# Kernel optimization log

Measured on AMD Instinct MI355X. Metric: run time of the kernel, lower is better.

Reference implementation:

```python
import jax, jax.numpy as jnp
from jax import lax
import numpy as np

B, N, H, K = 64, 256, 1024, 3  # batch, num_proposals, hidden_dim, conv kernel size
LN_EPS = 1e-5


def setup_inputs() -> dict:
    key = jax.random.key(0)
    k1, k2, k3 = jax.random.split(key, 3)
    scale = 1.0 / np.sqrt(H)
    return {
        "f": jax.random.normal(k1, (B, N, H), dtype=jnp.float32),
        "k": jax.random.normal(k2, (B, N, H), dtype=jnp.float32),
        "W_lin": jax.random.normal(k3, (N * K, H), dtype=jnp.float32) * scale,
        "b_lin": jnp.zeros((N * K,), dtype=jnp.float32),
        "ln_gamma": jnp.ones((H,), dtype=jnp.float32),
        "ln_beta": jnp.zeros((H,), dtype=jnp.float32),
    }


def _conv_one(x, w):
    # x: [N, H] (channels, length); w: [N_out, N_in, K]
    # PyTorch F.conv1d is cross-correlation, same as lax conv with no flip.
    y = lax.conv_general_dilated(
        x[None], w, window_strides=(1,), padding="SAME",
        dimension_numbers=("NCH", "OIH", "NCH"))
    return y[0]  # [N, H]


def reference(f, k, W_lin, b_lin, ln_gamma, ln_beta):
    # Dynamic weight generation: [B, N, H] -> [B, N, N*K] -> [B, N, N, K]
    weight = jnp.einsum("bnh,oh->bno", f, W_lin) + b_lin
    weight = weight.reshape(B, N, N, K)
    # Per-sample dynamic conv1d over the hidden dim (batched via vmap)
    out = jax.vmap(_conv_one)(k, weight)  # [B, N, H]
    # LayerNorm over hidden dim
    mu = jnp.mean(out, axis=-1, keepdims=True)
    var = jnp.var(out, axis=-1, keepdims=True)
    out = (out - mu) * lax.rsqrt(var + LN_EPS) * ln_gamma + ln_beta
    return out
```

## Files before the change

### kernel.cpp

```cpp
#include <hip/hip_runtime.h>
#include <math.h>

#define Bsz 64
#define Nn  256
#define Hh  1024
#define NK  768

typedef __bf16 bf16;
typedef bf16 bf16x4 __attribute__((ext_vector_type(4)));
typedef bf16 bf16x8 __attribute__((ext_vector_type(8)));
typedef float floatx4 __attribute__((ext_vector_type(4)));

#define KT_ROWS   1026
#define KT_BSTRIDE (KT_ROWS * 256)

__device__ __forceinline__ void gl_lds16(const bf16* g, bf16* l) {
    __builtin_amdgcn_global_load_lds(
        (__attribute__((address_space(1))) void*)(g),
        (__attribute__((address_space(3))) void*)(l), 16, 0, 0);
}
__device__ __forceinline__ void gl_lds16f(const float* g, float* l) {
    __builtin_amdgcn_global_load_lds(
        (__attribute__((address_space(1))) void*)(g),
        (__attribute__((address_space(3))) void*)(l), 16, 0, 0);
}

__global__ __launch_bounds__(256) void transpose_kernel(
    const float* __restrict__ kin, bf16* __restrict__ kTp)
{
    __shared__ float Tf[64 * 128];
    const int tid = threadIdx.x;
    const int bid = blockIdx.x;
    const int hb = bid & 7, ib = (bid >> 3) & 3, b = bid >> 5;
    const int i0 = ib * 64, h0 = hb * 128;
    const float* src = kin + ((size_t)b << 18);
    bf16* dstb = kTp + (size_t)b * KT_BSTRIDE;

    if (hb == 0 && ib == 0) {
        dstb[tid] = (bf16)0.f;
        dstb[(size_t)1025 * 256 + tid] = (bf16)0.f;
    }
    #pragma unroll
    for (int j = 0; j < 8; ++j) {
        int c  = tid + j * 256;
        int il = c >> 5;
        int hq = (c & 31) ^ j;
        gl_lds16f(src + (size_t)(i0 + il) * Hh + h0 + hq * 4, Tf + c * 4);
    }
    __syncthreads();
    const int q = tid & 7;
    #pragma unroll
    for (int p = 0; p < 4; ++p) {
        int hl = (tid >> 3) + p * 32;
        bf16x8 o;
        #pragma unroll
        for (int j = 0; j < 8; ++j) {
            int i = q * 8 + j;
            float v = Tf[i * 128 + (((hl >> 2) ^ q) << 2) + (hl & 3)];
            o[j] = (bf16)v;
        }
        *(bf16x8*)&dstb[(size_t)(h0 + hl + 1) * 256 + i0 + q * 8] = o;
    }
}

__global__ __launch_bounds__(256) void gemm1_mfma(
    const float* __restrict__ A,
    const float* __restrict__ Bw,
    const float* __restrict__ bias,
    bf16* __restrict__ wgt3)
{
    __shared__ bf16 smem[25600];
    const int tid  = threadIdx.x;
    const int wave = tid >> 6, lane = tid & 63;
    const int bid = blockIdx.x;
    const int xcd = bid & 7, loc = bid >> 3;
    const int ry  = (xcd << 4) | (loc >> 2);
    const int cx  = loc & 3;
    const int row0 = ry * 128;
    const int col0 = cx * 192;

    size_t offA[8];
    #pragma unroll
    for (int j = 0; j < 8; ++j) {
        int c = tid + j * 256, row = c >> 4, kq = c & 15;
        offA[j] = (size_t)(row0 + row) * Hh + kq * 4;
    }
    size_t offB[12];
    #pragma unroll
    for (int j = 0; j < 12; ++j) {
        int c = tid + j * 256, row = c >> 4, kq = c & 15;
        offB[j] = (size_t)(col0 + row) * Hh + kq * 4;
    }

    const int wm = wave & 1, wn = wave >> 1;
    const int fm = lane & 15, koct = (lane >> 4) * 8;

    floatx4 zero = {0.f, 0.f, 0.f, 0.f};
    floatx4 acc[4][6];
    #pragma unroll
    for (int i = 0; i < 4; ++i)
        #pragma unroll
        for (int j = 0; j < 6; ++j) acc[i][j] = zero;

    for (int k0 = 0; k0 < Hh; k0 += 64) {
        float4 av[8];
        #pragma unroll
        for (int j = 0; j < 8; ++j) av[j] = *(const float4*)&A[offA[j] + k0];
        float4 bv[12];
        #pragma unroll
        for (int j = 0; j < 12; ++j) bv[j] = *(const float4*)&Bw[offB[j] + k0];
        __syncthreads();
        #pragma unroll
        for (int j = 0; j < 8; ++j) {
            int c = tid + j * 256;
            bf16x4 o = {(bf16)av[j].x, (bf16)av[j].y, (bf16)av[j].z, (bf16)av[j].w};
            *(bf16x4*)&smem[c * 4] = o;
        }
        #pragma unroll
        for (int j = 0; j < 12; ++j) {
            int c = tid + j * 256;
            bf16x4 o = {(bf16)bv[j].x, (bf16)bv[j].y, (bf16)bv[j].z, (bf16)bv[j].w};
            *(bf16x4*)&smem[8192 + c * 4] = o;
        }
        __syncthreads();
        #pragma unroll
        for (int q = 0; q < 2; ++q) {
            bf16x8 af[4], bfr[6];
            #pragma unroll
            for (int mt = 0; mt < 4; ++mt)
                af[mt] = *(const bf16x8*)&smem[(wm * 64 + mt * 16 + fm) * 64 + q * 32 + koct];
            #pragma unroll
            for (int nt = 0; nt < 6; ++nt)
                bfr[nt] = *(const bf16x8*)&smem[8192 + (wn * 96 + nt * 16 + fm) * 64 + q * 32 + koct];
            #pragma unroll
            for (int mt = 0; mt < 4; ++mt)
                #pragma unroll
                for (int nt = 0; nt < 6; ++nt)
                    acc[mt][nt] = __builtin_amdgcn_mfma_f32_16x16x32_bf16(
                        af[mt], bfr[nt], acc[mt][nt], 0, 0, 0);
        }
    }
    __syncthreads();

    const int b  = row0 >> 8;
    const int nb = row0 & 255;
    bf16* Cs = smem;
    #pragma unroll
    for (int nt = 0; nt < 6; ++nt) {
        int c = wn * 96 + nt * 16 + fm;
        float bl = bias[col0 + c];
        #pragma unroll
        for (int mt = 0; mt < 4; ++mt) {
            int rb = wm * 64 + mt * 16 + (lane >> 4) * 4;
            #pragma unroll
            for (int r = 0; r < 4; ++r)
                Cs[(rb + r) * 200 + c] = (bf16)(acc[mt][nt][r] + bl);
        }
    }
    __syncthreads();
    const int i0 = cx * 64;
    #pragma unroll
    for (int j = 0; j < 12; ++j) {
        int s = tid + j * 256;
        int t = s >> 10, rem = s & 1023, n = rem >> 3, q8 = rem & 7;
        bf16x8 v;
        #pragma unroll
        for (int u = 0; u < 8; ++u)
            v[u] = Cs[n * 200 + (q8 * 8 + u) * 3 + t];
        *(bf16x8*)&wgt3[((size_t)(b * 3 + t) << 16) + ((size_t)(nb + n) << 8) + i0 + q8 * 8] = v;
    }
}

__global__ __launch_bounds__(256) void conv_mfma(
    const bf16* __restrict__ kTp,
    const bf16* __restrict__ wgt3,
    bf16* __restrict__ cbuf)
{
    __shared__ bf16 As[6144];
    __shared__ bf16 Ks[4160];
    const int tid  = threadIdx.x;
    const int wave = tid >> 6, lane = tid & 63;
    const int bid = blockIdx.x;
    const int xcd = bid & 7, loc = bid >> 3;
    const int b   = (xcd << 3) | (loc >> 5);
    const int rem = loc & 31;
    const int o0  = (rem >> 3) * 64;
    const int h0  = (rem & 7) * 128;
    const int wm = wave & 1, wn = wave >> 1;
    const int fm = lane & 15, koct = (lane >> 4) * 8;

    const bf16* gA[3]; bf16* lA[3];
    #pragma unroll
    for (int j = 0; j < 3; ++j) {
        int s = tid + j * 256;
        int t = s >> 8, r2 = s & 255, o = r2 >> 2, iq = r2 & 3;
        gA[j] = wgt3 + ((size_t)(b * 3 + t) << 16) + ((size_t)(o0 + o) << 8) + iq * 8;
        lA[j] = As + s * 8;
    }
    const bf16* kb = kTp + (size_t)b * KT_BSTRIDE;
    const bf16* gK[2]; bf16* lK[2];
    #pragma unroll
    for (int j = 0; j < 2; ++j) {
        int s = tid + j * 256;
        int r = s >> 2, quad = s & 3;
        gK[j] = kb + (size_t)(h0 + r) * 256 + quad * 8;
        lK[j] = Ks + s * 8;
    }
    const bf16* gH = kb + (size_t)(h0 + 128 + (tid >> 2)) * 256 + (tid & 3) * 8;
    const int lH = (128 + (tid >> 2)) * 32 + (tid & 3) * 8;

    floatx4 zero = {0.f, 0.f, 0.f, 0.f};
    floatx4 acc[2][4];
    #pragma unroll
    for (int i = 0; i < 2; ++i)
        #pragma unroll
        for (int j = 0; j < 4; ++j) acc[i][j] = zero;

    for (int ic = 0; ic < 8; ++ic) {
        const int i0 = ic * 32;
        __syncthreads();
        #pragma unroll
        for (int j = 0; j < 3; ++j) gl_lds16(gA[j] + i0, lA[j]);
        #pragma unroll
        for (int j = 0; j < 2; ++j) gl_lds16(gK[j] + i0, lK[j]);
        if (tid < 8) {
            bf16x8 v = *(const bf16x8*)(gH + i0);
            *(bf16x8*)&Ks[lH] = v;
        }
        __syncthreads();
        #pragma unroll
        for (int t = 0; t < 3; ++t) {
            bf16x8 af[2], bfr[4];
            #pragma unroll
            for (int mt = 0; mt < 2; ++mt)
                af[mt] = *(const bf16x8*)&As[t * 2048 + (wm * 32 + mt * 16 + fm) * 32 + koct];
            #pragma unroll
            for (int nt = 0; nt < 4; ++nt)
                bfr[nt] = *(const bf16x8*)&Ks[(wn * 64 + nt * 16 + fm + t) * 32 + koct];
            #pragma unroll
            for (int mt = 0; mt < 2; ++mt)
                #pragma unroll
                for (int nt = 0; nt < 4; ++nt)
                    acc[mt][nt] = __builtin_amdgcn_mfma_f32_16x16x32_bf16(
                        af[mt], bfr[nt], acc[mt][nt], 0, 0, 0);
        }
    }

    #pragma unroll
    for (int mt = 0; mt < 2; ++mt) {
        int o = o0 + wm * 32 + mt * 16 + (lane >> 4) * 4;
        #pragma unroll
        for (int nt = 0; nt < 4; ++nt) {
            int h = h0 + wn * 64 + nt * 16 + fm;
            #pragma unroll
            for (int r = 0; r < 4; ++r)
                cbuf[((size_t)(b * 256 + o + r) << 10) + h] = (bf16)acc[mt][nt][r];
        }
    }
}

__global__ __launch_bounds__(256) void ln_kernel(
    const bf16* __restrict__ cbuf, const float* __restrict__ gamma,
    const float* __restrict__ beta, float* __restrict__ out)
{
    const int tid  = threadIdx.x;
    const int t    = tid & 127;
    const int half = tid >> 7;
    bf16x8 v[4];
    #pragma unroll
    for (int it = 0; it < 4; ++it) {
        const int row = (blockIdx.x << 3) + it * 2 + half;
        v[it] = *(const bf16x8*)(cbuf + ((size_t)row << 10) + t * 8);
    }
    float4 g0  = ((const float4*)gamma)[t * 2];
    float4 g1  = ((const float4*)gamma)[t * 2 + 1];
    float4 be0 = ((const float4*)beta)[t * 2];
    float4 be1 = ((const float4*)beta)[t * 2 + 1];
    __shared__ float r1[2][4], r2[2][4];
    #pragma unroll
    for (int it = 0; it < 4; ++it) {
        const int row = (blockIdx.x << 3) + it * 2 + half;
        float x[8];
        float s1 = 0.f, s2 = 0.f;
        #pragma unroll
        for (int u = 0; u < 8; ++u) {
            x[u] = (float)v[it][u];
            s1 += x[u];
            s2 += x[u] * x[u];
        }
        #pragma unroll
        for (int m = 1; m < 64; m <<= 1) {
            s1 += __shfl_xor(s1, m, 64);
            s2 += __shfl_xor(s2, m, 64);
        }
        const int p = it & 1;
        if ((tid & 63) == 0) { r1[p][tid >> 6] = s1; r2[p][tid >> 6] = s2; }
        __syncthreads();
        float S1 = r1[p][2 * half] + r1[p][2 * half + 1];
        float S2 = r2[p][2 * half] + r2[p][2 * half + 1];
        float mu   = S1 * (1.0f / 1024.0f);
        float var  = S2 * (1.0f / 1024.0f) - mu * mu;
        float rstd = rsqrtf(var + 1e-5f);
        float4 o0, o1;
        o0.x = (x[0] - mu) * rstd * g0.x + be0.x;
        o0.y = (x[1] - mu) * rstd * g0.y + be0.y;
        o0.z = (x[2] - mu) * rstd * g0.z + be0.z;
        o0.w = (x[3] - mu) * rstd * g0.w + be0.w;
        o1.x = (x[4] - mu) * rstd * g1.x + be1.x;
        o1.y = (x[5] - mu) * rstd * g1.y + be1.y;
        o1.z = (x[6] - mu) * rstd * g1.z + be1.z;
        o1.w = (x[7] - mu) * rstd * g1.w + be1.w;
        float* orow = out + ((size_t)row << 10) + t * 8;
        ((float4*)orow)[0] = o0;
        ((float4*)orow)[1] = o1;
    }
}

extern "C" void kernel_launch(void* const* d_in, const int* in_sizes, int n_in,
                              void* d_out, int out_size, void* d_ws, size_t ws_size,
                              hipStream_t stream) {
    const float* f     = (const float*)d_in[0];
    const float* kin   = (const float*)d_in[1];
    const float* W_lin = (const float*)d_in[2];
    const float* b_lin = (const float*)d_in[3];
    const float* gamma = (const float*)d_in[4];
    const float* beta  = (const float*)d_in[5];
    float* out = (float*)d_out;

    char* ws = (char*)d_ws;
    bf16* cbuf = (bf16*)(ws);
    bf16* kTp  = (bf16*)(ws + 35127296);
    bf16* wgt3 = (bf16*)(ws + 68747264);

    transpose_kernel<<<2048, 256, 0, stream>>>(kin, kTp);
    gemm1_mfma<<<512, 256, 0, stream>>>(f, W_lin, b_lin, wgt3);
    conv_mfma<<<2048, 256, 0, stream>>>(kTp, wgt3, cbuf);
    ln_kernel<<<2048, 256, 0, stream>>>(cbuf, gamma, beta, out);
}
```

Measured before the change: 259.8 us.

## Double-buffer gemm1 LDS with register prefetch and halve the output tile

The weight-generation GEMM now uses a 128x96 output tile instead of 128x192, doubling the grid to 1024 blocks. The K loop steps by 32 instead of 64 and uses two LDS buffers: the next slice is prefetched into registers while MFMAs run on the current buffer, then stored to the other buffer, so each step needs one barrier instead of two. LDS rows are padded to a stride of 40 to reduce bank conflicts. Smaller tiles mean more global reloads of the A operand across column blocks, traded for better occupancy and latency hiding.

```diff
diff --git a/kernel.cpp b/kernel.cpp
--- a/kernel.cpp
+++ b/kernel.cpp
@@ -69,104 +69,123 @@
     const float* __restrict__ bias,
     bf16* __restrict__ wgt3)
 {
-    __shared__ bf16 smem[25600];
+    __shared__ bf16 smem[17920];
     const int tid  = threadIdx.x;
     const int wave = tid >> 6, lane = tid & 63;
     const int bid = blockIdx.x;
     const int xcd = bid & 7, loc = bid >> 3;
-    const int ry  = (xcd << 4) | (loc >> 2);
-    const int cx  = loc & 3;
+    const int ry  = (xcd << 4) | (loc >> 3);
+    const int cx  = loc & 7;
     const int row0 = ry * 128;
-    const int col0 = cx * 192;
-
-    size_t offA[8];
-    #pragma unroll
-    for (int j = 0; j < 8; ++j) {
-        int c = tid + j * 256, row = c >> 4, kq = c & 15;
-        offA[j] = (size_t)(row0 + row) * Hh + kq * 4;
-    }
-    size_t offB[12];
-    #pragma unroll
-    for (int j = 0; j < 12; ++j) {
-        int c = tid + j * 256, row = c >> 4, kq = c & 15;
-        offB[j] = (size_t)(col0 + row) * Hh + kq * 4;
+    const int col0 = cx * 96;
+
+    const float* gA[4]; int lA[4];
+    #pragma unroll
+    for (int j = 0; j < 4; ++j) {
+        int c = tid + j * 256, row = c >> 3, kq = c & 7;
+        gA[j] = A + (size_t)(row0 + row) * Hh + kq * 4;
+        lA[j] = row * 40 + kq * 4;
+    }
+    const float* gB[3]; int lB[3];
+    #pragma unroll
+    for (int j = 0; j < 3; ++j) {
+        int c = tid + j * 256, row = c >> 3, kq = c & 7;
+        gB[j] = Bw + (size_t)(col0 + row) * Hh + kq * 4;
+        lB[j] = 5120 + row * 40 + kq * 4;
     }
 
     const int wm = wave & 1, wn = wave >> 1;
     const int fm = lane & 15, koct = (lane >> 4) * 8;
 
     floatx4 zero = {0.f, 0.f, 0.f, 0.f};
-    floatx4 acc[4][6];
+    floatx4 acc[4][3];
     #pragma unroll
     for (int i = 0; i < 4; ++i)
         #pragma unroll
-        for (int j = 0; j < 6; ++j) acc[i][j] = zero;
-
-    for (int k0 = 0; k0 < Hh; k0 += 64) {
-        float4 av[8];
-        #pragma unroll
-        for (int j = 0; j < 8; ++j) av[j] = *(const float4*)&A[offA[j] + k0];
-        float4 bv[12];
-        #pragma unroll
-        for (int j = 0; j < 12; ++j) bv[j] = *(const float4*)&Bw[offB[j] + k0];
+        for (int j = 0; j < 3; ++j) acc[i][j] = zero;
+
+    float4 av[4]; float4 bv[3];
+    #pragma unroll
+    for (int j = 0; j < 4; ++j) av[j] = *(const float4*)(gA[j]);
+    #pragma unroll
+    for (int j = 0; j < 3; ++j) bv[j] = *(const float4*)(gB[j]);
+    #pragma unroll
+    for (int j = 0; j < 4; ++j) {
+        bf16x4 o = {(bf16)av[j].x, (bf16)av[j].y, (bf16)av[j].z, (bf16)av[j].w};
+        *(bf16x4*)&smem[lA[j]] = o;
+    }
+    #pragma unroll
+    for (int j = 0; j < 3; ++j) {
+        bf16x4 o = {(bf16)bv[j].x, (bf16)bv[j].y, (bf16)bv[j].z, (bf16)bv[j].w};
+        *(bf16x4*)&smem[lB[j]] = o;
+    }
+    __syncthreads();
+
+    int cur = 0;
+    for (int ks = 0; ks < 32; ++ks) {
+        if (ks < 31) {
+            const int ko = (ks + 1) * 32;
+            #pragma unroll
+            for (int j = 0; j < 4; ++j) av[j] = *(const float4*)(gA[j] + ko);
+            #pragma unroll
+            for (int j = 0; j < 3; ++j) bv[j] = *(const float4*)(gB[j] + ko);
+        }
+        const int cb = cur * 8960;
+        bf16x8 af[4], bfr[3];
+        #pragma unroll
+        for (int mt = 0; mt < 4; ++mt)
+            af[mt] = *(const bf16x8*)&smem[cb + (wm * 64 + mt * 16 + fm) * 40 + koct];
+        #pragma unroll
+        for (int nt = 0; nt < 3; ++nt)
+            bfr[nt] = *(const bf16x8*)&smem[cb + 5120 + (wn * 48 + nt * 16 + fm) * 40 + koct];
+        #pragma unroll
+        for (int mt = 0; mt < 4; ++mt)
+            #pragma unroll
+            for (int nt = 0; nt < 3; ++nt)
+                acc[mt][nt] = __builtin_amdgcn_mfma_f32_16x16x32_bf16(
+                    af[mt], bfr[nt], acc[mt][nt], 0, 0, 0);
+        if (ks < 31) {
+            const int ob = (cur ^ 1) * 8960;
+            #pragma unroll
+            for (int j = 0; j < 4; ++j) {
+                bf16x4 o = {(bf16)av[j].x, (bf16)av[j].y, (bf16)av[j].z, (bf16)av[j].w};
+                *(bf16x4*)&smem[ob + lA[j]] = o;
+            }
+            #pragma unroll
+            for (int j = 0; j < 3; ++j) {
+                bf16x4 o = {(bf16)bv[j].x, (bf16)bv[j].y, (bf16)bv[j].z, (bf16)bv[j].w};
+                *(bf16x4*)&smem[ob + lB[j]] = o;
+            }
+        }
         __syncthreads();
-        #pragma unroll
-        for (int j = 0; j < 8; ++j) {
-            int c = tid + j * 256;
-            bf16x4 o = {(bf16)av[j].x, (bf16)av[j].y, (bf16)av[j].z, (bf16)av[j].w};
-            *(bf16x4*)&smem[c * 4] = o;
-        }
-        #pragma unroll
-        for (int j = 0; j < 12; ++j) {
-            int c = tid + j * 256;
-            bf16x4 o = {(bf16)bv[j].x, (bf16)bv[j].y, (bf16)bv[j].z, (bf16)bv[j].w};
-            *(bf16x4*)&smem[8192 + c * 4] = o;
-        }
-        __syncthreads();
-        #pragma unroll
-        for (int q = 0; q < 2; ++q) {
-            bf16x8 af[4], bfr[6];
-            #pragma unroll
-            for (int mt = 0; mt < 4; ++mt)
-                af[mt] = *(const bf16x8*)&smem[(wm * 64 + mt * 16 + fm) * 64 + q * 32 + koct];
-            #pragma unroll
-            for (int nt = 0; nt < 6; ++nt)
-                bfr[nt] = *(const bf16x8*)&smem[8192 + (wn * 96 + nt * 16 + fm) * 64 + q * 32 + koct];
-            #pragma unroll
-            for (int mt = 0; mt < 4; ++mt)
-                #pragma unroll
-                for (int nt = 0; nt < 6; ++nt)
-                    acc[mt][nt] = __builtin_amdgcn_mfma_f32_16x16x32_bf16(
-                        af[mt], bfr[nt], acc[mt][nt], 0, 0, 0);
-        }
-    }
-    __syncthreads();
+        cur ^= 1;
+    }
 
     const int b  = row0 >> 8;
     const int nb = row0 & 255;
     bf16* Cs = smem;
     #pragma unroll
-    for (int nt = 0; nt < 6; ++nt) {
-        int c = wn * 96 + nt * 16 + fm;
+    for (int nt = 0; nt < 3; ++nt) {
+        int c = wn * 48 + nt * 16 + fm;
         float bl = bias[col0 + c];
         #pragma unroll
         for (int mt = 0; mt < 4; ++mt) {
             int rb = wm * 64 + mt * 16 + (lane >> 4) * 4;
             #pragma unroll
             for (int r = 0; r < 4; ++r)
-                Cs[(rb + r) * 200 + c] = (bf16)(acc[mt][nt][r] + bl);
+                Cs[(rb + r) * 104 + c] = (bf16)(acc[mt][nt][r] + bl);
         }
     }
     __syncthreads();
-    const int i0 = cx * 64;
-    #pragma unroll
-    for (int j = 0; j < 12; ++j) {
+    const int i0 = cx * 32;
+    #pragma unroll
+    for (int j = 0; j < 6; ++j) {
         int s = tid + j * 256;
-        int t = s >> 10, rem = s & 1023, n = rem >> 3, q8 = rem & 7;
+        int t = s >> 9, rem = s & 511, n = rem >> 2, q8 = rem & 3;
         bf16x8 v;
         #pragma unroll
         for (int u = 0; u < 8; ++u)
-            v[u] = Cs[n * 200 + (q8 * 8 + u) * 3 + t];
+            v[u] = Cs[n * 104 + (q8 * 8 + u) * 3 + t];
         *(bf16x8*)&wgt3[((size_t)(b * 3 + t) << 16) + ((size_t)(nb + n) << 8) + i0 + q8 * 8] = v;
     }
 }
@@ -333,7 +352,7 @@
     bf16* wgt3 = (bf16*)(ws + 68747264);
 
     transpose_kernel<<<2048, 256, 0, stream>>>(kin, kTp);
-    gemm1_mfma<<<512, 256, 0, stream>>>(f, W_lin, b_lin, wgt3);
+    gemm1_mfma<<<1024, 256, 0, stream>>>(f, W_lin, b_lin, wgt3);
     conv_mfma<<<2048, 256, 0, stream>>>(kTp, wgt3, cbuf);
     ln_kernel<<<2048, 256, 0, stream>>>(cbuf, gamma, beta, out);
 }
```

Measured after the change: 284.7 us. 9.6% more time.

## Prefetch next K-tile into registers and pad LDS rows in gemm1

Applied to the files above, without the earlier changes.

Restructures the gemm1 main loop so the global loads for the next 64-wide K slice are issued before the MFMA work on the current slice. This hides global memory latency behind compute at the cost of holding more live registers. It also pads the LDS row stride from 64 to 72 bf16 and changes the epilogue stride from 200 to 194, both meant to cut LDS bank conflicts. The LDS footprint grows, and the added registers could reduce occupancy.

```diff
diff --git a/kernel.cpp b/kernel.cpp
--- a/kernel.cpp
+++ b/kernel.cpp
@@ -79,17 +79,19 @@
     const int row0 = ry * 128;
     const int col0 = cx * 192;
 
-    size_t offA[8];
+    const float* gA[8]; int lA[8];
     #pragma unroll
     for (int j = 0; j < 8; ++j) {
         int c = tid + j * 256, row = c >> 4, kq = c & 15;
-        offA[j] = (size_t)(row0 + row) * Hh + kq * 4;
-    }
-    size_t offB[12];
+        gA[j] = A + (size_t)(row0 + row) * Hh + kq * 4;
+        lA[j] = row * 72 + kq * 4;
+    }
+    const float* gB[12]; int lB[12];
     #pragma unroll
     for (int j = 0; j < 12; ++j) {
         int c = tid + j * 256, row = c >> 4, kq = c & 15;
-        offB[j] = (size_t)(col0 + row) * Hh + kq * 4;
+        gB[j] = Bw + (size_t)(col0 + row) * Hh + kq * 4;
+        lB[j] = 9216 + row * 72 + kq * 4;
     }
 
     const int wm = wave & 1, wn = wave >> 1;
@@ -102,36 +104,41 @@
         #pragma unroll
         for (int j = 0; j < 6; ++j) acc[i][j] = zero;
 
-    for (int k0 = 0; k0 < Hh; k0 += 64) {
-        float4 av[8];
-        #pragma unroll
-        for (int j = 0; j < 8; ++j) av[j] = *(const float4*)&A[offA[j] + k0];
-        float4 bv[12];
-        #pragma unroll
-        for (int j = 0; j < 12; ++j) bv[j] = *(const float4*)&Bw[offB[j] + k0];
-        __syncthreads();
-        #pragma unroll
-        for (int j = 0; j < 8; ++j) {
-            int c = tid + j * 256;
-            bf16x4 o = {(bf16)av[j].x, (bf16)av[j].y, (bf16)av[j].z, (bf16)av[j].w};
-            *(bf16x4*)&smem[c * 4] = o;
-        }
-        #pragma unroll
-        for (int j = 0; j < 12; ++j) {
-            int c = tid + j * 256;
-            bf16x4 o = {(bf16)bv[j].x, (bf16)bv[j].y, (bf16)bv[j].z, (bf16)bv[j].w};
-            *(bf16x4*)&smem[8192 + c * 4] = o;
-        }
-        __syncthreads();
+    float4 av[8]; float4 bv[12];
+    #pragma unroll
+    for (int j = 0; j < 8; ++j) av[j] = *(const float4*)(gA[j]);
+    #pragma unroll
+    for (int j = 0; j < 12; ++j) bv[j] = *(const float4*)(gB[j]);
+    #pragma unroll
+    for (int j = 0; j < 8; ++j) {
+        bf16x4 o = {(bf16)av[j].x, (bf16)av[j].y, (bf16)av[j].z, (bf16)av[j].w};
+        *(bf16x4*)&smem[lA[j]] = o;
+    }
+    #pragma unroll
+    for (int j = 0; j < 12; ++j) {
+        bf16x4 o = {(bf16)bv[j].x, (bf16)bv[j].y, (bf16)bv[j].z, (bf16)bv[j].w};
+        *(bf16x4*)&smem[lB[j]] = o;
+    }
+    __syncthreads();
+
+    for (int ks = 0; ks < 16; ++ks) {
+        if (ks < 15) {
+            const int ko = (ks + 1) * 64;
+            #pragma unroll
+            for (int j = 0; j < 8; ++j) av[j] = *(const float4*)(gA[j] + ko);
+            #pragma unroll
+            for (int j = 0; j < 12; ++j) bv[j] = *(const float4*)(gB[j] + ko);
+            __builtin_amdgcn_sched_barrier(0);
+        }
         #pragma unroll
         for (int q = 0; q < 2; ++q) {
             bf16x8 af[4], bfr[6];
             #pragma unroll
             for (int mt = 0; mt < 4; ++mt)
-                af[mt] = *(const bf16x8*)&smem[(wm * 64 + mt * 16 + fm) * 64 + q * 32 + koct];
+                af[mt] = *(const bf16x8*)&smem[(wm * 64 + mt * 16 + fm) * 72 + q * 32 + koct];
             #pragma unroll
             for (int nt = 0; nt < 6; ++nt)
-                bfr[nt] = *(const bf16x8*)&smem[8192 + (wn * 96 + nt * 16 + fm) * 64 + q * 32 + koct];
+                bfr[nt] = *(const bf16x8*)&smem[9216 + (wn * 96 + nt * 16 + fm) * 72 + q * 32 + koct];
             #pragma unroll
             for (int mt = 0; mt < 4; ++mt)
                 #pragma unroll
@@ -139,6 +146,20 @@
                     acc[mt][nt] = __builtin_amdgcn_mfma_f32_16x16x32_bf16(
                         af[mt], bfr[nt], acc[mt][nt], 0, 0, 0);
         }
+        __syncthreads();
+        if (ks < 15) {
+            #pragma unroll
+            for (int j = 0; j < 8; ++j) {
+                bf16x4 o = {(bf16)av[j].x, (bf16)av[j].y, (bf16)av[j].z, (bf16)av[j].w};
+                *(bf16x4*)&smem[lA[j]] = o;
+            }
+            #pragma unroll
+            for (int j = 0; j < 12; ++j) {
+                bf16x4 o = {(bf16)bv[j].x, (bf16)bv[j].y, (bf16)bv[j].z, (bf16)bv[j].w};
+                *(bf16x4*)&smem[lB[j]] = o;
+            }
+            __syncthreads();
+        }
     }
     __syncthreads();
 
@@ -154,7 +175,7 @@
             int rb = wm * 64 + mt * 16 + (lane >> 4) * 4;
             #pragma unroll
             for (int r = 0; r < 4; ++r)
-                Cs[(rb + r) * 200 + c] = (bf16)(acc[mt][nt][r] + bl);
+                Cs[(rb + r) * 194 + c] = (bf16)(acc[mt][nt][r] + bl);
         }
     }
     __syncthreads();
@@ -166,7 +187,7 @@
         bf16x8 v;
         #pragma unroll
         for (int u = 0; u < 8; ++u)
-            v[u] = Cs[n * 200 + (q8 * 8 + u) * 3 + t];
+            v[u] = Cs[n * 194 + (q8 * 8 + u) * 3 + t];
         *(bf16x8*)&wgt3[((size_t)(b * 3 + t) << 16) + ((size_t)(nb + n) << 8) + i0 + q8 * 8] = v;
     }
 }
```

After: 297.6 us. 14.6% more time.
